# Optimization experiments

Hardware: AMD Instinct MI355X
Metric: run time of the kernel (lower is better)

Reference implementation:

```python
import jax, jax.numpy as jnp
import numpy as np

N = 100000        # nodes
E = 1600000       # edges (avg degree 16)
D_IN = 128        # input_dim
HID = 128         # hidden
L = 2             # num_layers
EPS = 1e-5        # LayerNorm eps (torch default)


def setup_inputs() -> dict:
    key = jax.random.key(0)
    ks = jax.random.split(key, 5)
    x = jax.random.normal(ks[0], (N, D_IN), dtype=jnp.float32)
    edge_index = jax.random.randint(ks[1], (2, E), 0, N, dtype=jnp.int64)
    e_feat = jax.random.uniform(ks[2], (E,), dtype=jnp.float32)
    # nn.Linear(input_dim, hidden): weight [hidden, input_dim], bias [hidden]
    lin_w = jax.random.normal(ks[3], (HID, D_IN), dtype=jnp.float32) / np.float32(np.sqrt(D_IN))
    lin_b = jax.random.normal(ks[4], (HID,), dtype=jnp.float32) * 0.01
    ln_scale = jnp.ones((L, HID), dtype=jnp.float32)
    ln_bias = jnp.zeros((L, HID), dtype=jnp.float32)
    return {"x": x, "edge_index": edge_index, "e_feat": e_feat,
            "lin_w": lin_w, "lin_b": lin_b,
            "ln_scale": ln_scale, "ln_bias": ln_bias}


def _layernorm(h, scale, bias):
    mu = jnp.mean(h, axis=-1, keepdims=True)
    var = jnp.mean(jnp.square(h - mu), axis=-1, keepdims=True)
    return (h - mu) * jax.lax.rsqrt(var + EPS) * scale + bias


def reference(x, edge_index, e_feat, lin_w, lin_b, ln_scale, ln_bias):
    src, dst = edge_index[0], edge_index[1]
    h = x @ lin_w.T + lin_b            # [N, HID]
    ori = h
    for i in range(L):
        if i != 0:                      # res=True
            h = h + ori
        h = _layernorm(h, ln_scale[i], ln_bias[i])   # norm=True
        h = jax.nn.relu(h)              # relu=True; dp=0 -> dropout no-op
        # GraphConv(weight=False, bias=False): weighted SpMM aggregation
        msg = h[src] * e_feat[:, None]  # [E, HID]
        h = jax.ops.segment_sum(msg, dst, num_segments=N)  # [N, HID]
    return h
```

## Files before the change

### kernel.cpp

```cpp
#include <hip/hip_runtime.h>


constexpr int N_NODES = 100000;
constexpr int N_EDGES = 1600000;
constexpr int HID     = 128;
constexpr int NBKT    = (N_NODES + 511) / 512;
constexpr int BCAP    = 9216;
constexpr float LN_EPS = 1e-5f;

typedef __attribute__((ext_vector_type(8))) short short8;
typedef __attribute__((ext_vector_type(4))) float floatx4;

__device__ inline unsigned pack_bf16x2(float a, float b) {
    unsigned ua = __float_as_uint(a), ub = __float_as_uint(b);
    ua += 0x7fff + ((ua >> 16) & 1);
    ub += 0x7fff + ((ub >> 16) & 1);
    return (ua >> 16) | (ub & 0xffff0000u);
}

__global__ void k_prepw(const float* __restrict__ W, unsigned* __restrict__ Wb) {
    int i = blockIdx.x * 256 + threadIdx.x;
    float2 w = ((const float2*)W)[i];
    Wb[i] = pack_bf16x2(w.x, w.y);
}

__global__ __launch_bounds__(256) void k_bin(const int* __restrict__ ei,
                                             const float* __restrict__ ef,
                                             int* __restrict__ gcur,
                                             int* __restrict__ gbufDst,
                                             int2* __restrict__ gbufSW) {
    __shared__ int cnt[NBKT];
    __shared__ int incl[256];
    __shared__ int gbase[NBKT];
    __shared__ int sdst[2048];
    __shared__ int2 ssw[2048];
    const int t = threadIdx.x;

    for (int e0 = blockIdx.x * 2048; e0 < N_EDGES; e0 += gridDim.x * 2048) {
        for (int i = t; i < NBKT; i += 256) cnt[i] = 0;
        __syncthreads();

        const int nE = min(2048, N_EDGES - e0);
        int ed[8], es[8], ep[8]; float ew[8];
        const int base = e0 + t * 8;
        if (base + 8 <= N_EDGES) {
            int4 s0 = *(const int4*)&ei[base];
            int4 s1 = *(const int4*)&ei[base + 4];
            int4 d0 = *(const int4*)&ei[N_EDGES + base];
            int4 d1 = *(const int4*)&ei[N_EDGES + base + 4];
            float4 w0 = *(const float4*)&ef[base];
            float4 w1 = *(const float4*)&ef[base + 4];
            es[0]=s0.x; es[1]=s0.y; es[2]=s0.z; es[3]=s0.w;
            es[4]=s1.x; es[5]=s1.y; es[6]=s1.z; es[7]=s1.w;
            ed[0]=d0.x; ed[1]=d0.y; ed[2]=d0.z; ed[3]=d0.w;
            ed[4]=d1.x; ed[5]=d1.y; ed[6]=d1.z; ed[7]=d1.w;
            ew[0]=w0.x; ew[1]=w0.y; ew[2]=w0.z; ew[3]=w0.w;
            ew[4]=w1.x; ew[5]=w1.y; ew[6]=w1.z; ew[7]=w1.w;
#pragma unroll
            for (int k = 0; k < 8; ++k) ep[k] = atomicAdd(&cnt[ed[k] >> 9], 1);
        } else {
#pragma unroll
            for (int k = 0; k < 8; ++k) {
                int idx = base + k;
                if (idx < N_EDGES) {
                    es[k] = ei[idx]; ed[k] = ei[N_EDGES + idx]; ew[k] = ef[idx];
                    ep[k] = atomicAdd(&cnt[ed[k] >> 9], 1);
                } else ed[k] = -1;
            }
        }
        __syncthreads();

        int v = (t < NBKT) ? cnt[t] : 0;
        incl[t] = v;
        for (int o = 1; o < 256; o <<= 1) {
            __syncthreads();
            int u = (t >= o) ? incl[t - o] : 0;
            __syncthreads();
            incl[t] += u;
        }
        __syncthreads();
        if (t < NBKT) gbase[t] = atomicAdd(&gcur[t], v);
        __syncthreads();

#pragma unroll
        for (int k = 0; k < 8; ++k) {
            if (ed[k] < 0) continue;
            int b = ed[k] >> 9;
            int idx = incl[b] - cnt[b] + ep[k];
            sdst[idx] = ed[k];
            ssw[idx] = make_int2(es[k], __float_as_int(ew[k]));
        }
        __syncthreads();

        for (int j = t; j < nE; j += 256) {
            int d = sdst[j];
            int b = d >> 9;
            int pos = gbase[b] + (j - (incl[b] - cnt[b]));
            if (pos < BCAP) {
                gbufDst[(size_t)b * BCAP + pos] = d;
                gbufSW [(size_t)b * BCAP + pos] = ssw[j];
            }
        }
        __syncthreads();
    }
}

__global__ __launch_bounds__(256) void k_scan(const int* __restrict__ gcur,
                                              int* __restrict__ cbase,
                                              int* __restrict__ rp) {
    __shared__ int s[256];
    const int t = threadIdx.x;
    int v = (t < NBKT) ? min(gcur[t], BCAP) : 0;
    s[t] = v;
    for (int o = 1; o < 256; o <<= 1) {
        __syncthreads();
        int u = (t >= o) ? s[t - o] : 0;
        __syncthreads();
        s[t] += u;
    }
    __syncthreads();
    if (t < NBKT) cbase[t] = s[t] - v;
    if (t == NBKT - 1) rp[N_NODES] = s[t];
}

__global__ __launch_bounds__(512) void k_build(const int* __restrict__ gcur,
                                               const int* __restrict__ cbase,
                                               const int* __restrict__ gbufDst,
                                               const int2* __restrict__ gbufSW,
                                               int* __restrict__ rp,
                                               int2* __restrict__ csr) {
    __shared__ int cnt[512];
    __shared__ int cur[512];
    __shared__ int2 sorted[BCAP];
    const int t     = threadIdx.x;
    const int b     = blockIdx.x;
    const int nbase = b * 512;
    const int nb = min(gcur[b], BCAP);
    const int cb = cbase[b];
    const int*  bd = gbufDst + (size_t)b * BCAP;
    const int2* bs = gbufSW  + (size_t)b * BCAP;

    cnt[t] = 0;
    __syncthreads();
    for (int i = t; i < nb; i += 512) atomicAdd(&cnt[bd[i] - nbase], 1);
    __syncthreads();

    int v = cnt[t];
    for (int o = 1; o < 512; o <<= 1) {
        __syncthreads();
        int u = (t >= o) ? cnt[t - o] : 0;
        __syncthreads();
        cnt[t] += u;
    }
    __syncthreads();
    const int excl = cnt[t] - v;
    cur[t] = excl;
    if (nbase + t < N_NODES) rp[nbase + t] = cb + excl;
    __syncthreads();

    for (int i = t; i < nb; i += 512) {
        int d = bd[i];
        int pos = atomicAdd(&cur[d - nbase], 1);
        sorted[pos] = bs[i];
    }
    __syncthreads();
    for (int i = t; i < nb; i += 512) csr[(size_t)cb + i] = sorted[i];
}

__global__ __launch_bounds__(256) void k_gemm_mfma(const float* __restrict__ x,
                                                   const unsigned* __restrict__ Wb,
                                                   const float* __restrict__ bias,
                                                   const float* __restrict__ lns,
                                                   const float* __restrict__ lnb,
                                                   float* __restrict__ h0,
                                                   unsigned* __restrict__ hact) {
    __shared__ __align__(16) char smem[128 * 136 * 2 + 64 * 136 * 2];
    ushort (*Ws)[136] = (ushort(*)[136])smem;
    ushort (*Xs)[136] = (ushort(*)[136])(smem + 128 * 136 * 2);
    float  (*Hs)[132] = (float(*)[132])smem;

    const int t    = threadIdx.x;
    const int row0 = blockIdx.x * 64;

    {
        const uint4* Wg = (const uint4*)Wb;
#pragma unroll
        for (int i = 0; i < 8; ++i) {
            int g = t + 256 * i;
            int r = g >> 4;
            int c = (g & 15) * 8;
            uint4 vv = Wg[g];
            *(uint4*)&Ws[r][c] = vv;
        }
    }
    {
        const float4* xg = (const float4*)x;
        const int base = blockIdx.x * 2048;
#pragma unroll
        for (int i = 0; i < 8; ++i) {
            int f = t + 256 * i;
            int g = base + f;
            float4 vv = make_float4(0.f, 0.f, 0.f, 0.f);
            if (g < N_NODES * 32) vv = xg[g];
            int r = f >> 5;
            int c = (f & 31) * 4;
            uint2 p = make_uint2(pack_bf16x2(vv.x, vv.y), pack_bf16x2(vv.z, vv.w));
            *(uint2*)&Xs[r][c] = p;
        }
    }
    __syncthreads();

    const int wv   = t >> 6;
    const int l    = t & 63;
    const int mrow = l & 15;
    const int kq   = l >> 4;

    floatx4 acc[8];
#pragma unroll
    for (int i = 0; i < 8; ++i) acc[i] = (floatx4){0.f, 0.f, 0.f, 0.f};

#pragma unroll
    for (int ks = 0; ks < 4; ++ks) {
        short8 a = *(const short8*)&Xs[wv * 16 + mrow][ks * 32 + kq * 8];
#pragma unroll
        for (int tc = 0; tc < 8; ++tc) {
            short8 bb = *(const short8*)&Ws[tc * 16 + mrow][ks * 32 + kq * 8];
            acc[tc] = __builtin_amdgcn_mfma_f32_16x16x32_bf16(a, bb, acc[tc], 0, 0, 0);
        }
    }
    __syncthreads();

#pragma unroll
    for (int tc = 0; tc < 8; ++tc)
#pragma unroll
        for (int r = 0; r < 4; ++r)
            Hs[wv * 16 + kq * 4 + r][tc * 16 + mrow] = acc[tc][r];
    __syncthreads();

    const float2 b2  = ((const float2*)bias)[l];
    const float2 sc2 = ((const float2*)lns)[l];
    const float2 bb2 = ((const float2*)lnb)[l];
    for (int rr = 0; rr < 16; ++rr) {
        const int lrow = wv * 16 + rr;
        const int grow = row0 + lrow;
        if (grow >= N_NODES) break;
        float2 vv = *(const float2*)&Hs[lrow][l * 2];
        vv.x += b2.x; vv.y += b2.y;
        ((float2*)h0)[(size_t)grow * 64 + l] = vv;
        float s  = vv.x + vv.y;
        float s2 = vv.x * vv.x + vv.y * vv.y;
#pragma unroll
        for (int m = 1; m < 64; m <<= 1) {
            s  += __shfl_xor(s, m);
            s2 += __shfl_xor(s2, m);
        }
        const float mu   = s * (1.0f / 128.0f);
        const float var  = s2 * (1.0f / 128.0f) - mu * mu;
        const float rstd = rsqrtf(var + LN_EPS);
        float y0 = fmaxf((vv.x - mu) * rstd * sc2.x + bb2.x, 0.0f);
        float y1 = fmaxf((vv.y - mu) * rstd * sc2.y + bb2.y, 0.0f);
        hact[(size_t)grow * 64 + l] = pack_bf16x2(y0, y1);
    }
}

__global__ __launch_bounds__(256) void k_spmm_ln(const int* __restrict__ rp,
                                                 const int2* __restrict__ cw,
                                                 const unsigned* __restrict__ Hb,
                                                 const float* __restrict__ ori,
                                                 const float* __restrict__ lns,
                                                 const float* __restrict__ lnb,
                                                 unsigned* __restrict__ hout) {
    const int wid  = (blockIdx.x * 256 + threadIdx.x) >> 6;
    const int lane = threadIdx.x & 63;

    const int beg = __builtin_amdgcn_readfirstlane(rp[wid]);
    const int end = __builtin_amdgcn_readfirstlane(rp[wid + 1]);

    float2 acc = make_float2(0.0f, 0.0f);
    int e = beg;
    for (; e + 4 <= end; e += 4) {
        int2 c0 = cw[e], c1 = cw[e + 1], c2 = cw[e + 2], c3 = cw[e + 3];
        unsigned v0 = Hb[(size_t)c0.x * 64 + lane];
        unsigned v1 = Hb[(size_t)c1.x * 64 + lane];
        unsigned v2 = Hb[(size_t)c2.x * 64 + lane];
        unsigned v3 = Hb[(size_t)c3.x * 64 + lane];
        float w0 = __int_as_float(c0.y), w1 = __int_as_float(c1.y);
        float w2 = __int_as_float(c2.y), w3 = __int_as_float(c3.y);
        acc.x += w0 * __uint_as_float(v0 << 16) + w1 * __uint_as_float(v1 << 16)
               + w2 * __uint_as_float(v2 << 16) + w3 * __uint_as_float(v3 << 16);
        acc.y += w0 * __uint_as_float(v0 & 0xffff0000u) + w1 * __uint_as_float(v1 & 0xffff0000u)
               + w2 * __uint_as_float(v2 & 0xffff0000u) + w3 * __uint_as_float(v3 & 0xffff0000u);
    }
    for (; e < end; ++e) {
        int2 c0 = cw[e];
        unsigned v0 = Hb[(size_t)c0.x * 64 + lane];
        float w0 = __int_as_float(c0.y);
        acc.x += w0 * __uint_as_float(v0 << 16);
        acc.y += w0 * __uint_as_float(v0 & 0xffff0000u);
    }

    float2 o = ((const float2*)ori)[(size_t)wid * 64 + lane];
    float vx = acc.x + o.x, vy = acc.y + o.y;
    float s  = vx + vy;
    float s2 = vx * vx + vy * vy;
#pragma unroll
    for (int m = 1; m < 64; m <<= 1) {
        s  += __shfl_xor(s, m);
        s2 += __shfl_xor(s2, m);
    }
    const float mu   = s * (1.0f / 128.0f);
    const float var  = s2 * (1.0f / 128.0f) - mu * mu;
    const float rstd = rsqrtf(var + LN_EPS);
    const int c = lane * 2;
    float y0 = fmaxf((vx - mu) * rstd * lns[c]     + lnb[c],     0.0f);
    float y1 = fmaxf((vy - mu) * rstd * lns[c + 1] + lnb[c + 1], 0.0f);
    hout[(size_t)wid * 64 + lane] = pack_bf16x2(y0, y1);
}

__global__ __launch_bounds__(256) void k_spmm_out(const int* __restrict__ rp,
                                                  const int2* __restrict__ cw,
                                                  const unsigned* __restrict__ Hb,
                                                  float* __restrict__ out) {
    const int wid  = (blockIdx.x * 256 + threadIdx.x) >> 6;
    const int lane = threadIdx.x & 63;

    const int beg = __builtin_amdgcn_readfirstlane(rp[wid]);
    const int end = __builtin_amdgcn_readfirstlane(rp[wid + 1]);

    float2 acc = make_float2(0.0f, 0.0f);
    int e = beg;
    for (; e + 4 <= end; e += 4) {
        int2 c0 = cw[e], c1 = cw[e + 1], c2 = cw[e + 2], c3 = cw[e + 3];
        unsigned v0 = Hb[(size_t)c0.x * 64 + lane];
        unsigned v1 = Hb[(size_t)c1.x * 64 + lane];
        unsigned v2 = Hb[(size_t)c2.x * 64 + lane];
        unsigned v3 = Hb[(size_t)c3.x * 64 + lane];
        float w0 = __int_as_float(c0.y), w1 = __int_as_float(c1.y);
        float w2 = __int_as_float(c2.y), w3 = __int_as_float(c3.y);
        acc.x += w0 * __uint_as_float(v0 << 16) + w1 * __uint_as_float(v1 << 16)
               + w2 * __uint_as_float(v2 << 16) + w3 * __uint_as_float(v3 << 16);
        acc.y += w0 * __uint_as_float(v0 & 0xffff0000u) + w1 * __uint_as_float(v1 & 0xffff0000u)
               + w2 * __uint_as_float(v2 & 0xffff0000u) + w3 * __uint_as_float(v3 & 0xffff0000u);
    }
    for (; e < end; ++e) {
        int2 c0 = cw[e];
        unsigned v0 = Hb[(size_t)c0.x * 64 + lane];
        float w0 = __int_as_float(c0.y);
        acc.x += w0 * __uint_as_float(v0 << 16);
        acc.y += w0 * __uint_as_float(v0 & 0xffff0000u);
    }
    ((float2*)out)[(size_t)wid * 64 + lane] = acc;
}

extern "C" void kernel_launch(void* const* d_in, const int* in_sizes, int n_in,
                              void* d_out, int out_size, void* d_ws, size_t ws_size,
                              hipStream_t stream) {
    const float* x   = (const float*)d_in[0];
    const int*   ei  = (const int*)d_in[1];
    const float* ef  = (const float*)d_in[2];
    const float* W   = (const float*)d_in[3];
    const float* b   = (const float*)d_in[4];
    const float* lns = (const float*)d_in[5];
    const float* lnb = (const float*)d_in[6];
    float* out = (float*)d_out;
    float* h0  = out;

    unsigned* hact  = (unsigned*)d_ws;
    unsigned* hact2 = hact + (size_t)N_NODES * 64;
    int2* csr    = (int2*)(hact2 + (size_t)N_NODES * 64);
    int2* gbufSW = csr + N_EDGES;
    unsigned* Wb = (unsigned*)(gbufSW + (size_t)NBKT * BCAP);
    int* gcur    = (int*)(Wb + 8192);
    int* cbase   = gcur + NBKT;
    int* rp      = cbase + NBKT;
    int* gbufDst = rp + (N_NODES + 1);

    const int wb = N_NODES * 64 / 256;

    hipMemsetAsync(gcur, 0, NBKT * sizeof(int), stream);
    k_prepw<<<32, 256, 0, stream>>>(W, Wb);
    k_bin<<<256, 256, 0, stream>>>(ei, ef, gcur, gbufDst, gbufSW);
    k_scan<<<1, 256, 0, stream>>>(gcur, cbase, rp);
    k_build<<<NBKT, 512, 0, stream>>>(gcur, cbase, gbufDst, gbufSW, rp, csr);

    k_gemm_mfma<<<(N_NODES + 63) / 64, 256, 0, stream>>>(x, Wb, b, lns, lnb, h0, hact);

    k_spmm_ln<<<wb, 256, 0, stream>>>(rp, csr, hact, h0, lns + HID, lnb + HID, hact2);
    k_spmm_out<<<wb, 256, 0, stream>>>(rp, csr, hact2, out);
}
```

Before: 323.0 us.

## Fuse prep kernels, store residual in bf16, process two nodes per wave in SpMM

Folds the weight bf16 conversion into the GEMM kernel and the bucket prefix scan into the CSR build kernel, removing two launches. The residual activation is stored as bf16 in the output buffer instead of fp32, halving its write and read traffic. The SpMM kernels now assign half a wave per node with 8-byte gathers, looping to the pair's max degree with masked weights. This reduces per-lane load count but adds redundant scans per block and bf16 rounding of the residual.

```diff
diff --git a/kernel.cpp b/kernel.cpp
--- a/kernel.cpp
+++ b/kernel.cpp
@@ -17,12 +17,8 @@
     ub += 0x7fff + ((ub >> 16) & 1);
     return (ua >> 16) | (ub & 0xffff0000u);
 }
-
-__global__ void k_prepw(const float* __restrict__ W, unsigned* __restrict__ Wb) {
-    int i = blockIdx.x * 256 + threadIdx.x;
-    float2 w = ((const float2*)W)[i];
-    Wb[i] = pack_bf16x2(w.x, w.y);
-}
+__device__ inline float bflo(unsigned u) { return __uint_as_float(u << 16); }
+__device__ inline float bfhi(unsigned u) { return __uint_as_float(u & 0xffff0000u); }
 
 __global__ __launch_bounds__(256) void k_bin(const int* __restrict__ ei,
                                              const float* __restrict__ ef,
@@ -105,26 +101,7 @@
     }
 }
 
-__global__ __launch_bounds__(256) void k_scan(const int* __restrict__ gcur,
-                                              int* __restrict__ cbase,
-                                              int* __restrict__ rp) {
-    __shared__ int s[256];
-    const int t = threadIdx.x;
-    int v = (t < NBKT) ? min(gcur[t], BCAP) : 0;
-    s[t] = v;
-    for (int o = 1; o < 256; o <<= 1) {
-        __syncthreads();
-        int u = (t >= o) ? s[t - o] : 0;
-        __syncthreads();
-        s[t] += u;
-    }
-    __syncthreads();
-    if (t < NBKT) cbase[t] = s[t] - v;
-    if (t == NBKT - 1) rp[N_NODES] = s[t];
-}
-
 __global__ __launch_bounds__(512) void k_build(const int* __restrict__ gcur,
-                                               const int* __restrict__ cbase,
                                                const int* __restrict__ gbufDst,
                                                const int2* __restrict__ gbufSW,
                                                int* __restrict__ rp,
@@ -135,8 +112,21 @@
     const int t     = threadIdx.x;
     const int b     = blockIdx.x;
     const int nbase = b * 512;
+
+    int v0 = (t < NBKT) ? min(gcur[t], BCAP) : 0;
+    cnt[t] = v0;
+    for (int o = 1; o < 512; o <<= 1) {
+        __syncthreads();
+        int u = (t >= o) ? cnt[t - o] : 0;
+        __syncthreads();
+        cnt[t] += u;
+    }
+    __syncthreads();
     const int nb = min(gcur[b], BCAP);
-    const int cb = cbase[b];
+    const int cb = cnt[b] - nb;
+    if (b == NBKT - 1 && t == 0) rp[N_NODES] = cnt[NBKT - 1];
+    __syncthreads();
+
     const int*  bd = gbufDst + (size_t)b * BCAP;
     const int2* bs = gbufSW  + (size_t)b * BCAP;
 
@@ -168,11 +158,11 @@
 }
 
 __global__ __launch_bounds__(256) void k_gemm_mfma(const float* __restrict__ x,
-                                                   const unsigned* __restrict__ Wb,
+                                                   const float* __restrict__ W,
                                                    const float* __restrict__ bias,
                                                    const float* __restrict__ lns,
                                                    const float* __restrict__ lnb,
-                                                   float* __restrict__ h0,
+                                                   unsigned* __restrict__ orib,
                                                    unsigned* __restrict__ hact) {
     __shared__ __align__(16) char smem[128 * 136 * 2 + 64 * 136 * 2];
     ushort (*Ws)[136] = (ushort(*)[136])smem;
@@ -183,13 +173,15 @@
     const int row0 = blockIdx.x * 64;
 
     {
-        const uint4* Wg = (const uint4*)Wb;
+        const float4* Wf = (const float4*)W;
 #pragma unroll
         for (int i = 0; i < 8; ++i) {
             int g = t + 256 * i;
+            float4 p = Wf[g * 2], q = Wf[g * 2 + 1];
+            uint4 vv = make_uint4(pack_bf16x2(p.x, p.y), pack_bf16x2(p.z, p.w),
+                                  pack_bf16x2(q.x, q.y), pack_bf16x2(q.z, q.w));
             int r = g >> 4;
             int c = (g & 15) * 8;
-            uint4 vv = Wg[g];
             *(uint4*)&Ws[r][c] = vv;
         }
     }
@@ -246,7 +238,7 @@
         if (grow >= N_NODES) break;
         float2 vv = *(const float2*)&Hs[lrow][l * 2];
         vv.x += b2.x; vv.y += b2.y;
-        ((float2*)h0)[(size_t)grow * 64 + l] = vv;
+        orib[(size_t)grow * 64 + l] = pack_bf16x2(vv.x, vv.y);
         float s  = vv.x + vv.y;
         float s2 = vv.x * vv.x + vv.y * vv.y;
 #pragma unroll
@@ -263,93 +255,91 @@
     }
 }
 
+__device__ inline void spmm_body(const int* __restrict__ rp,
+                                 const int2* __restrict__ csr,
+                                 const uint2* __restrict__ H2,
+                                 int n, int l32, int deg, int beg, int maxd,
+                                 float& a0, float& a1, float& a2, float& a3) {
+    for (int j = 0; j < maxd; j += 4) {
+#pragma unroll
+        for (int k = 0; k < 4; ++k) {
+            const int jj = j + k;
+            const bool valid = jj < deg;
+            const int idx = valid ? beg + jj : 0;
+            int2 c = csr[idx];
+            float w = valid ? __int_as_float(c.y) : 0.0f;
+            uint2 v = H2[(size_t)c.x * 32 + l32];
+            a0 += w * bflo(v.x);
+            a1 += w * bfhi(v.x);
+            a2 += w * bflo(v.y);
+            a3 += w * bfhi(v.y);
+        }
+    }
+}
+
 __global__ __launch_bounds__(256) void k_spmm_ln(const int* __restrict__ rp,
-                                                 const int2* __restrict__ cw,
+                                                 const int2* __restrict__ csr,
                                                  const unsigned* __restrict__ Hb,
-                                                 const float* __restrict__ ori,
+                                                 const unsigned* __restrict__ orib,
                                                  const float* __restrict__ lns,
                                                  const float* __restrict__ lnb,
                                                  unsigned* __restrict__ hout) {
     const int wid  = (blockIdx.x * 256 + threadIdx.x) >> 6;
     const int lane = threadIdx.x & 63;
-
-    const int beg = __builtin_amdgcn_readfirstlane(rp[wid]);
-    const int end = __builtin_amdgcn_readfirstlane(rp[wid + 1]);
-
-    float2 acc = make_float2(0.0f, 0.0f);
-    int e = beg;
-    for (; e + 4 <= end; e += 4) {
-        int2 c0 = cw[e], c1 = cw[e + 1], c2 = cw[e + 2], c3 = cw[e + 3];
-        unsigned v0 = Hb[(size_t)c0.x * 64 + lane];
-        unsigned v1 = Hb[(size_t)c1.x * 64 + lane];
-        unsigned v2 = Hb[(size_t)c2.x * 64 + lane];
-        unsigned v3 = Hb[(size_t)c3.x * 64 + lane];
-        float w0 = __int_as_float(c0.y), w1 = __int_as_float(c1.y);
-        float w2 = __int_as_float(c2.y), w3 = __int_as_float(c3.y);
-        acc.x += w0 * __uint_as_float(v0 << 16) + w1 * __uint_as_float(v1 << 16)
-               + w2 * __uint_as_float(v2 << 16) + w3 * __uint_as_float(v3 << 16);
-        acc.y += w0 * __uint_as_float(v0 & 0xffff0000u) + w1 * __uint_as_float(v1 & 0xffff0000u)
-               + w2 * __uint_as_float(v2 & 0xffff0000u) + w3 * __uint_as_float(v3 & 0xffff0000u);
-    }
-    for (; e < end; ++e) {
-        int2 c0 = cw[e];
-        unsigned v0 = Hb[(size_t)c0.x * 64 + lane];
-        float w0 = __int_as_float(c0.y);
-        acc.x += w0 * __uint_as_float(v0 << 16);
-        acc.y += w0 * __uint_as_float(v0 & 0xffff0000u);
-    }
-
-    float2 o = ((const float2*)ori)[(size_t)wid * 64 + lane];
-    float vx = acc.x + o.x, vy = acc.y + o.y;
-    float s  = vx + vy;
-    float s2 = vx * vx + vy * vy;
-#pragma unroll
-    for (int m = 1; m < 64; m <<= 1) {
+    const int half = lane >> 5;
+    const int l32  = lane & 31;
+    const int n    = wid * 2 + half;
+
+    const int beg = rp[n];
+    const int deg = rp[n + 1] - beg;
+    int maxd = deg;
+    maxd = max(maxd, __shfl_xor(maxd, 32));
+
+    float a0 = 0.f, a1 = 0.f, a2 = 0.f, a3 = 0.f;
+    spmm_body(rp, csr, (const uint2*)Hb, n, l32, deg, beg, maxd, a0, a1, a2, a3);
+
+    uint2 o = ((const uint2*)orib)[(size_t)n * 32 + l32];
+    float v0 = a0 + bflo(o.x), v1 = a1 + bfhi(o.x);
+    float v2 = a2 + bflo(o.y), v3 = a3 + bfhi(o.y);
+    float s  = v0 + v1 + v2 + v3;
+    float s2 = v0 * v0 + v1 * v1 + v2 * v2 + v3 * v3;
+#pragma unroll
+    for (int m = 1; m < 32; m <<= 1) {
         s  += __shfl_xor(s, m);
         s2 += __shfl_xor(s2, m);
     }
     const float mu   = s * (1.0f / 128.0f);
     const float var  = s2 * (1.0f / 128.0f) - mu * mu;
     const float rstd = rsqrtf(var + LN_EPS);
-    const int c = lane * 2;
-    float y0 = fmaxf((vx - mu) * rstd * lns[c]     + lnb[c],     0.0f);
-    float y1 = fmaxf((vy - mu) * rstd * lns[c + 1] + lnb[c + 1], 0.0f);
-    hout[(size_t)wid * 64 + lane] = pack_bf16x2(y0, y1);
+    const float4 sc = ((const float4*)lns)[l32];
+    const float4 bb = ((const float4*)lnb)[l32];
+    float y0 = fmaxf((v0 - mu) * rstd * sc.x + bb.x, 0.0f);
+    float y1 = fmaxf((v1 - mu) * rstd * sc.y + bb.y, 0.0f);
+    float y2 = fmaxf((v2 - mu) * rstd * sc.z + bb.z, 0.0f);
+    float y3 = fmaxf((v3 - mu) * rstd * sc.w + bb.w, 0.0f);
+    ((uint2*)hout)[(size_t)n * 32 + l32] =
+        make_uint2(pack_bf16x2(y0, y1), pack_bf16x2(y2, y3));
 }
 
 __global__ __launch_bounds__(256) void k_spmm_out(const int* __restrict__ rp,
-                                                  const int2* __restrict__ cw,
+                                                  const int2* __restrict__ csr,
                                                   const unsigned* __restrict__ Hb,
                                                   float* __restrict__ out) {
     const int wid  = (blockIdx.x * 256 + threadIdx.x) >> 6;
     const int lane = threadIdx.x & 63;
-
-    const int beg = __builtin_amdgcn_readfirstlane(rp[wid]);
-    const int end = __builtin_amdgcn_readfirstlane(rp[wid + 1]);
-
-    float2 acc = make_float2(0.0f, 0.0f);
-    int e = beg;
-    for (; e + 4 <= end; e += 4) {
-        int2 c0 = cw[e], c1 = cw[e + 1], c2 = cw[e + 2], c3 = cw[e + 3];
-        unsigned v0 = Hb[(size_t)c0.x * 64 + lane];
-        unsigned v1 = Hb[(size_t)c1.x * 64 + lane];
-        unsigned v2 = Hb[(size_t)c2.x * 64 + lane];
-        unsigned v3 = Hb[(size_t)c3.x * 64 + lane];
-        float w0 = __int_as_float(c0.y), w1 = __int_as_float(c1.y);
-        float w2 = __int_as_float(c2.y), w3 = __int_as_float(c3.y);
-        acc.x += w0 * __uint_as_float(v0 << 16) + w1 * __uint_as_float(v1 << 16)
-               + w2 * __uint_as_float(v2 << 16) + w3 * __uint_as_float(v3 << 16);
-        acc.y += w0 * __uint_as_float(v0 & 0xffff0000u) + w1 * __uint_as_float(v1 & 0xffff0000u)
-               + w2 * __uint_as_float(v2 & 0xffff0000u) + w3 * __uint_as_float(v3 & 0xffff0000u);
-    }
-    for (; e < end; ++e) {
-        int2 c0 = cw[e];
-        unsigned v0 = Hb[(size_t)c0.x * 64 + lane];
-        float w0 = __int_as_float(c0.y);
-        acc.x += w0 * __uint_as_float(v0 << 16);
-        acc.y += w0 * __uint_as_float(v0 & 0xffff0000u);
-    }
-    ((float2*)out)[(size_t)wid * 64 + lane] = acc;
+    const int half = lane >> 5;
+    const int l32  = lane & 31;
+    const int n    = wid * 2 + half;
+
+    const int beg = rp[n];
+    const int deg = rp[n + 1] - beg;
+    int maxd = deg;
+    maxd = max(maxd, __shfl_xor(maxd, 32));
+
+    float a0 = 0.f, a1 = 0.f, a2 = 0.f, a3 = 0.f;
+    spmm_body(rp, csr, (const uint2*)Hb, n, l32, deg, beg, maxd, a0, a1, a2, a3);
+
+    ((float4*)out)[(size_t)n * 32 + l32] = make_float4(a0, a1, a2, a3);
 }
 
 extern "C" void kernel_launch(void* const* d_in, const int* in_sizes, int n_in,
@@ -363,28 +353,25 @@
     const float* lns = (const float*)d_in[5];
     const float* lnb = (const float*)d_in[6];
     float* out = (float*)d_out;
-    float* h0  = out;
+
+    unsigned* orib = (unsigned*)d_out;
 
     unsigned* hact  = (unsigned*)d_ws;
     unsigned* hact2 = hact + (size_t)N_NODES * 64;
     int2* csr    = (int2*)(hact2 + (size_t)N_NODES * 64);
     int2* gbufSW = csr + N_EDGES;
-    unsigned* Wb = (unsigned*)(gbufSW + (size_t)NBKT * BCAP);
-    int* gcur    = (int*)(Wb + 8192);
-    int* cbase   = gcur + NBKT;
-    int* rp      = cbase + NBKT;
+    int* gcur    = (int*)(gbufSW + (size_t)NBKT * BCAP);
+    int* rp      = gcur + NBKT;
     int* gbufDst = rp + (N_NODES + 1);
 
-    const int wb = N_NODES * 64 / 256;
+    const int sb = N_NODES / 2 * 64 / 256;
 
     hipMemsetAsync(gcur, 0, NBKT * sizeof(int), stream);
-    k_prepw<<<32, 256, 0, stream>>>(W, Wb);
     k_bin<<<256, 256, 0, stream>>>(ei, ef, gcur, gbufDst, gbufSW);
-    k_scan<<<1, 256, 0, stream>>>(gcur, cbase, rp);
-    k_build<<<NBKT, 512, 0, stream>>>(gcur, cbase, gbufDst, gbufSW, rp, csr);
-
-    k_gemm_mfma<<<(N_NODES + 63) / 64, 256, 0, stream>>>(x, Wb, b, lns, lnb, h0, hact);
-
-    k_spmm_ln<<<wb, 256, 0, stream>>>(rp, csr, hact, h0, lns + HID, lnb + HID, hact2);
-    k_spmm_out<<<wb, 256, 0, stream>>>(rp, csr, hact2, out);
-}
+    k_build<<<NBKT, 512, 0, stream>>>(gcur, gbufDst, gbufSW, rp, csr);
+
+    k_gemm_mfma<<<(N_NODES + 63) / 64, 256, 0, stream>>>(x, W, b, lns, lnb, orib, hact);
+
+    k_spmm_ln<<<sb, 256, 0, stream>>>(rp, csr, hact, orib, lns + HID, lnb + HID, hact2);
+    k_spmm_out<<<sb, 256, 0, stream>>>(rp, csr, hact2, out);
+}
```

New measurement: 353.3 us. 1.09x slower.
